# Optimization experiments

Measured on AMD Instinct MI355X. Metric: run time of the kernel, lower is better.

Reference implementation:

```python
import jax, jax.numpy as jnp
import numpy as np

N_BOTTLENECK = 256  # must be a power of two for the butterfly network


def butterfly_ortho(x, theta, first_output_entry_positive=False):
    """FFT-like butterfly of Givens rotations over the last dim (size n, power of 2).
    Stage s pairs indices (i, i + 2^s); each pair gets one rotation angle.
    theta has (n/2)*log2(n) entries, consumed stage by stage.
    """
    n = x.shape[-1]
    stages = int(np.log2(n))
    idx = 0
    for s in range(stages):
        stride = 1 << s
        nb = n // (2 * stride)
        th = theta[idx: idx + n // 2].reshape(nb, stride)
        idx += n // 2
        xr = x.reshape(-1, nb, 2, stride)  # [B, blocks, half, offset]
        a, b = xr[:, :, 0, :], xr[:, :, 1, :]
        c, sn = jnp.cos(th), jnp.sin(th)
        a2 = c * a - sn * b
        b2 = sn * a + c * b
        x = jnp.stack([a2, b2], axis=2).reshape(-1, n)
    if first_output_entry_positive:
        # convention flag: force sign of first output entry non-negative
        x = x.at[:, 0].set(jnp.abs(x[:, 0]))
    return x


def setup_inputs() -> dict:
    key = jax.random.key(0)
    ks = jax.random.split(key, 12)
    dims = [4096, 1024, 256, 1024, 4096]
    B = 16384

    def w(k, i, o):
        return (jax.random.normal(k, (i, o), dtype=jnp.float32) * (1.0 / np.sqrt(i)))

    inp = {
        "x": jax.random.normal(ks[0], (B, dims[0]), dtype=jnp.float32),
        "enc_w0": w(ks[1], dims[0], dims[1]),
        "enc_b0": jnp.zeros((dims[1],), jnp.float32),
        "enc_w1": w(ks[2], dims[1], dims[2]),
        "enc_b1": jnp.zeros((dims[2],), jnp.float32),
        "theta": jax.random.normal(ks[3], ((dims[2] // 2) * int(np.log2(dims[2])),), dtype=jnp.float32),
        "dec_w0": w(ks[4], dims[2], dims[3]),
        "dec_b0": jnp.zeros((dims[3],), jnp.float32),
        "out_w": w(ks[5], dims[3], dims[4]),
        "out_b": jnp.zeros((dims[4],), jnp.float32),
    }
    return inp


def reference(x, enc_w0, enc_b0, enc_w1, enc_b1, theta, dec_w0, dec_b0, out_w, out_b):
    # encoder: Linear + ReLU stack
    h = jax.nn.relu(x @ enc_w0 + enc_b0)
    h = jax.nn.relu(h @ enc_w1 + enc_b1)
    # orthogonal butterfly network at the bottleneck
    h = butterfly_ortho(h, theta, first_output_entry_positive=False)
    # decoder: Linear + ReLU stack, then plain Linear output layer
    h = jax.nn.relu(h @ dec_w0 + dec_b0)
    out = h @ out_w + out_b
    return out
```

## Files before the change

### kernel.cpp

```cpp
#include <hip/hip_runtime.h>

typedef __attribute__((ext_vector_type(8))) short short8v;
typedef __attribute__((ext_vector_type(4))) float f32x4;
typedef __attribute__((ext_vector_type(4))) unsigned int uint4v;
typedef __attribute__((ext_vector_type(4))) float float4v;

__device__ __forceinline__ unsigned short f2bf(float f) {
  union { float f; unsigned u; } v; v.f = f;
  unsigned r = v.u + 0x7fffu + ((v.u >> 16) & 1u);
  return (unsigned short)(r >> 16);
}
__device__ __forceinline__ float bf2f(unsigned short h) {
  union { unsigned u; float f; } v; v.u = ((unsigned)h) << 16;
  return v.f;
}
__device__ __forceinline__ unsigned pack2(float a, float b) {
  return (unsigned)f2bf(a) | ((unsigned)f2bf(b) << 16);
}

__device__ __forceinline__ void gload_lds16(const void* g, void* l) {
  __builtin_amdgcn_global_load_lds(
      (const __attribute__((address_space(1))) void*)g,
      (__attribute__((address_space(3))) void*)l, 16, 0, 0);
}

#define SBAR() __builtin_amdgcn_s_barrier()
#define LGKM0() do { asm volatile("s_waitcnt lgkmcnt(0)" ::: "memory"); \
                     __builtin_amdgcn_sched_barrier(0); } while (0)
#define VMW4() asm volatile("s_waitcnt vmcnt(4)" ::: "memory")

__global__ void f32_to_bf16(const float* __restrict__ in, unsigned short* __restrict__ out,
                            size_t n8) {
  size_t i = (size_t)blockIdx.x * blockDim.x + threadIdx.x;
  const size_t stride = (size_t)gridDim.x * blockDim.x;
  for (; i < n8; i += stride) {
    const float4v* p = (const float4v*)(in + i * 8);
    float4v a = p[0], b = p[1];
    uint4v r;
    r.x = pack2(a.x, a.y); r.y = pack2(a.z, a.w);
    r.z = pack2(b.x, b.y); r.w = pack2(b.z, b.w);
    *(uint4v*)(out + i * 8) = r;
  }
}

__global__ void transpose_bf16(const float* __restrict__ W, unsigned short* __restrict__ WT,
                               int K, int N) {
  __shared__ float t[32][33];
  const int kb = blockIdx.x * 32, nb = blockIdx.y * 32;
  const int tx = threadIdx.x, ty = threadIdx.y;
  #pragma unroll
  for (int y = 0; y < 4; ++y)
    t[ty + y*8][tx] = W[(size_t)(kb + ty + y*8) * N + nb + tx];
  __syncthreads();
  #pragma unroll
  for (int y = 0; y < 4; ++y) {
    const int n = nb + ty + y*8;
    WT[(size_t)n * K + kb + tx] = f2bf(t[tx][ty + y*8]);
  }
}

__global__ void trig_kernel(const float* __restrict__ theta, float* __restrict__ ct,
                            float* __restrict__ st, int n) {
  const int i = blockIdx.x * 256 + threadIdx.x;
  if (i < n) {
    float s, c;
    sincosf(theta[i], &s, &c);
    ct[i] = c; st[i] = s;
  }
}

__global__ void butterfly_kernel(const unsigned short* __restrict__ X,
                                 unsigned short* __restrict__ Y,
                                 const float* __restrict__ ct, const float* __restrict__ st) {
  __shared__ float L[2][256];
  const int tid = threadIdx.x;
  const size_t base = (size_t)blockIdx.x * 512;
  const unsigned v = *(const unsigned*)(X + base + tid * 2);
  const int r = tid >> 7;
  const int col = (tid * 2) & 255;
  L[r][col]     = bf2f((unsigned short)(v & 0xffffu));
  L[r][col + 1] = bf2f((unsigned short)(v >> 16));
  __syncthreads();
  const int p = tid & 127;
  #pragma unroll
  for (int s = 0; s < 8; ++s) {
    const int stride = 1 << s;
    const int t = p & (stride - 1);
    const int i = ((p >> s) << (s + 1)) + t;
    const int j = i + stride;
    const float c  = ct[s * 128 + p];
    const float sn = st[s * 128 + p];
    const float a = L[r][i], b = L[r][j];
    L[r][i] = c * a - sn * b;
    L[r][j] = sn * a + c * b;
    __syncthreads();
  }
  const unsigned lo = f2bf(L[r][col]);
  const unsigned hi = f2bf(L[r][col + 1]);
  *(unsigned*)(Y + base + tid * 2) = lo | (hi << 16);
}

template<bool RELU, bool OUT_F32>
__global__ __launch_bounds__(256) void gemm_kernel(
    const unsigned short* __restrict__ A, const unsigned short* __restrict__ BT,
    const float* __restrict__ bias, void* __restrict__ Cp,
    int M, int N, int K)
{
  __shared__ __align__(16) unsigned short As[128 * 32];
  __shared__ __align__(16) unsigned short Bs[128 * 32];
  const int tid = threadIdx.x;
  const int lane = tid & 63;
  const int w = tid >> 6;
  const int wm = w >> 1, wn = w & 1;
  const int n0 = blockIdx.x * 128;
  const int m0 = blockIdx.y * 128;
  const int g4 = lane >> 4;
  const int ml = lane & 15;

  f32x4 acc[4][4];
  #pragma unroll
  for (int i = 0; i < 4; ++i)
    #pragma unroll
    for (int n = 0; n < 4; ++n)
      #pragma unroll
      for (int e = 0; e < 4; ++e)
        acc[i][n][e] = 0.0f;

  const int nkt = K >> 5;
  const int srow = w * 32 + (lane >> 2);
  const int scol = (lane & 3) * 8;

  for (int kt = 0; kt < nkt; ++kt) {
    const int k0 = kt << 5;
    #pragma unroll
    for (int q = 0; q < 2; ++q) {
      const unsigned short* gb = BT + (size_t)(n0 + srow + q * 16) * K + k0 + scol;
      gload_lds16(gb, Bs + w * 1024 + q * 512);
      const unsigned short* ga = A + (size_t)(m0 + srow + q * 16) * K + k0 + scol;
      gload_lds16(ga, As + w * 1024 + q * 512);
    }
    __syncthreads();
    short8v af[4], bf[4];
    #pragma unroll
    for (int i = 0; i < 4; ++i)
      af[i] = *(const short8v*)(As + (wm * 64 + i * 16 + ml) * 32 + g4 * 8);
    #pragma unroll
    for (int n = 0; n < 4; ++n)
      bf[n] = *(const short8v*)(Bs + (wn * 64 + n * 16 + ml) * 32 + g4 * 8);
    #pragma unroll
    for (int i = 0; i < 4; ++i)
      #pragma unroll
      for (int n = 0; n < 4; ++n)
        acc[i][n] = __builtin_amdgcn_mfma_f32_16x16x32_bf16(af[i], bf[n], acc[i][n], 0, 0, 0);
    __syncthreads();
  }
  #pragma unroll
  for (int n = 0; n < 4; ++n) {
    const int col = n0 + wn * 64 + n * 16 + ml;
    const float bv = bias[col];
    #pragma unroll
    for (int i = 0; i < 4; ++i) {
      const int rowb = m0 + wm * 64 + i * 16 + g4 * 4;
      #pragma unroll
      for (int r = 0; r < 4; ++r) {
        float v = acc[i][n][r] + bv;
        if constexpr (RELU) v = fmaxf(v, 0.0f);
        if constexpr (OUT_F32)
          ((float*)Cp)[(size_t)(rowb + r) * N + col] = v;
        else
          ((unsigned short*)Cp)[(size_t)(rowb + r) * N + col] = f2bf(v);
      }
    }
  }
}

template<int MI0, int NI0>
__device__ __forceinline__ void mfma_quad(f32x4 (&acc)[8][4], const short8v (&a)[4][2],
                                          const short8v (&b)[2][2]) {
  __builtin_amdgcn_s_setprio(1);
  #pragma unroll
  for (int mi = 0; mi < 4; ++mi)
    #pragma unroll
    for (int ni = 0; ni < 2; ++ni) {
      acc[MI0+mi][NI0+ni] = __builtin_amdgcn_mfma_f32_16x16x32_bf16(
          a[mi][0], b[ni][0], acc[MI0+mi][NI0+ni], 0, 0, 0);
      acc[MI0+mi][NI0+ni] = __builtin_amdgcn_mfma_f32_16x16x32_bf16(
          a[mi][1], b[ni][1], acc[MI0+mi][NI0+ni], 0, 0, 0);
    }
  __builtin_amdgcn_s_setprio(0);
}

template<bool RELU, bool OUT_F32>
__global__ __launch_bounds__(512, 2) void gemm256(
    const unsigned short* __restrict__ A, const unsigned short* __restrict__ BT,
    const float* __restrict__ bias, void* __restrict__ Cp,
    int M, int N, int K)
{
  __shared__ __align__(16) unsigned char lds[131072];
  const int tid = threadIdx.x;
  const int lane = tid & 63, w = tid >> 6;
  const int wm = w >> 2, wn = w & 3;
  const int ml = lane & 15, g4 = lane >> 4;

  const int nx = gridDim.x;
  const int nwg = nx * (int)gridDim.y;
  const int bid = blockIdx.y * nx + blockIdx.x;
  const int cpx = nwg >> 3;
  const int swz = (bid & 7) * cpx + (bid >> 3);
  const int n0 = (swz % nx) * 256;
  const int m0 = (swz / nx) * 256;

  const int rloc = w * 8 + (lane >> 3);
  const int scol = ((lane & 7) ^ (lane >> 3)) * 8;
  const int ldst = w * 1024;

  const int off0 = (g4 * 16) ^ ((ml & 7) << 4);
  const int aoff = (wm * 128 + ml) * 128 + off0;
  const int boff = (wn * 64 + ml) * 128 + off0;

  const int NT = K >> 6;
  const int NJ = NT >> 1;

  f32x4 acc[8][4];
  #pragma unroll
  for (int mi = 0; mi < 8; ++mi)
    #pragma unroll
    for (int ni = 0; ni < 4; ++ni)
      #pragma unroll
      for (int e = 0; e < 4; ++e)
        acc[mi][ni][e] = 0.0f;

  auto stA = [&](int d, int h, int t) {
    const unsigned short* g0 = A + (size_t)(m0 + h * 128 + rloc) * K + t * 64 + scol;
    unsigned char* l0 = lds + d * 65536 + h * 16384 + ldst;
    gload_lds16(g0, l0);
    gload_lds16(g0 + (size_t)64 * K, l0 + 8192);
  };
  auto stB = [&](int d, int h, int t) {
    const unsigned short* g0 = BT + (size_t)(n0 + h * 128 + rloc) * K + t * 64 + scol;
    unsigned char* l0 = lds + d * 65536 + 32768 + h * 16384 + ldst;
    gload_lds16(g0, l0);
    gload_lds16(g0 + (size_t)64 * K, l0 + 8192);
  };
  auto rdA = [&](short8v (&dst)[4][2], int d, int mh) {
    #pragma unroll
    for (int mi = 0; mi < 4; ++mi) {
      const int ab = d * 65536 + aoff + (mh * 4 + mi) * 2048;
      dst[mi][0] = *(const short8v*)(lds + ab);
      dst[mi][1] = *(const short8v*)(lds + (ab ^ 64));
    }
  };
  auto rdB = [&](short8v (&dst)[2][2], int d, int nh) {
    #pragma unroll
    for (int ni = 0; ni < 2; ++ni) {
      const int bb = d * 65536 + 32768 + boff + (nh * 2 + ni) * 2048;
      dst[ni][0] = *(const short8v*)(lds + bb);
      dst[ni][1] = *(const short8v*)(lds + (bb ^ 64));
    }
  };

  stB(0, 0, 0); stB(0, 1, 0); stA(0, 0, 0); stA(0, 1, 0);
  stB(1, 0, 1); stB(1, 1, 1);
  VMW4();
  SBAR();

  short8v aR[4][2], aR2[4][2], bR0[2][2], bR1[2][2];

  for (int j = 0; j < NJ; ++j) {
    const int t1 = 2 * j + 1;
    const int t2 = (2 * j + 2 < NT) ? 2 * j + 2 : NT - 1;
    const int t3 = (2 * j + 3 < NT) ? 2 * j + 3 : NT - 1;

    rdA(aR, 0, 0); rdB(bR0, 0, 0);
    stA(1, 0, t1);
    SBAR(); LGKM0();
    mfma_quad<0, 0>(acc, aR, bR0);
    SBAR();
    rdB(bR1, 0, 1);
    stA(1, 1, t1);
    SBAR(); LGKM0();
    mfma_quad<0, 2>(acc, aR, bR1);
    SBAR();
    rdA(aR2, 0, 1);
    stB(0, 0, t2);
    SBAR(); LGKM0();
    mfma_quad<4, 0>(acc, aR2, bR0);
    SBAR();
    stB(0, 1, t2);
    SBAR();
    mfma_quad<4, 2>(acc, aR2, bR1);
    VMW4();
    SBAR();
    rdA(aR, 1, 0); rdB(bR0, 1, 0);
    stA(0, 0, t2);
    SBAR(); LGKM0();
    mfma_quad<0, 0>(acc, aR, bR0);
    SBAR();
    rdB(bR1, 1, 1);
    stA(0, 1, t2);
    SBAR(); LGKM0();
    mfma_quad<0, 2>(acc, aR, bR1);
    SBAR();
    rdA(aR2, 1, 1);
    stB(1, 0, t3);
    SBAR(); LGKM0();
    mfma_quad<4, 0>(acc, aR2, bR0);
    SBAR();
    stB(1, 1, t3);
    SBAR();
    mfma_quad<4, 2>(acc, aR2, bR1);
    VMW4();
    SBAR();
  }

  #pragma unroll
  for (int ni = 0; ni < 4; ++ni) {
    const int col = n0 + wn * 64 + ni * 16 + ml;
    const float bv = bias[col];
    #pragma unroll
    for (int mi = 0; mi < 8; ++mi) {
      const int rowb = m0 + wm * 128 + mi * 16 + g4 * 4;
      #pragma unroll
      for (int r = 0; r < 4; ++r) {
        float v = acc[mi][ni][r] + bv;
        if constexpr (RELU) v = fmaxf(v, 0.0f);
        if constexpr (OUT_F32)
          ((float*)Cp)[(size_t)(rowb + r) * N + col] = v;
        else
          ((unsigned short*)Cp)[(size_t)(rowb + r) * N + col] = f2bf(v);
      }
    }
  }
}

extern "C" void kernel_launch(void* const* d_in, const int* in_sizes, int n_in,
                              void* d_out, int out_size, void* d_ws, size_t ws_size,
                              hipStream_t stream) {
  const float* x      = (const float*)d_in[0];
  const float* enc_w0 = (const float*)d_in[1];
  const float* enc_b0 = (const float*)d_in[2];
  const float* enc_w1 = (const float*)d_in[3];
  const float* enc_b1 = (const float*)d_in[4];
  const float* theta  = (const float*)d_in[5];
  const float* dec_w0 = (const float*)d_in[6];
  const float* dec_b0 = (const float*)d_in[7];
  const float* out_w  = (const float*)d_in[8];
  const float* out_b  = (const float*)d_in[9];
  float* out = (float*)d_out;

  char* ws = (char*)d_ws;
  unsigned short* xb  = (unsigned short*)(ws);
  unsigned short* wt0 = (unsigned short*)(ws + 134217728);
  unsigned short* wt1 = (unsigned short*)(ws + 142606336);
  unsigned short* wt2 = (unsigned short*)(ws + 143130624);
  unsigned short* wt3 = (unsigned short*)(ws + 143654912);
  unsigned short* h1  = (unsigned short*)(ws + 152043520);
  unsigned short* h2  = (unsigned short*)(ws + 185597952);
  unsigned short* h2b = (unsigned short*)(ws + 193986560);
  unsigned short* h3  = h1;
  float* ct = (float*)(ws + 202375168);
  float* st = ct + 1024;

  const int B = 16384;

  f32_to_bf16<<<2048, 256, 0, stream>>>(x, xb, (size_t)B * 4096 / 8);
  transpose_bf16<<<dim3(4096/32, 1024/32), dim3(32, 8), 0, stream>>>(enc_w0, wt0, 4096, 1024);
  transpose_bf16<<<dim3(1024/32,  256/32), dim3(32, 8), 0, stream>>>(enc_w1, wt1, 1024, 256);
  transpose_bf16<<<dim3( 256/32, 1024/32), dim3(32, 8), 0, stream>>>(dec_w0, wt2, 256, 1024);
  transpose_bf16<<<dim3(1024/32, 4096/32), dim3(32, 8), 0, stream>>>(out_w,  wt3, 1024, 4096);
  trig_kernel<<<4, 256, 0, stream>>>(theta, ct, st, 1024);

  gemm256<true,  false><<<dim3(1024/256, B/256), 512, 0, stream>>>(xb, wt0, enc_b0, h1, B, 1024, 4096);
  gemm_kernel<true,  false><<<dim3( 256/128, B/128), 256, 0, stream>>>(h1, wt1, enc_b1, h2, B, 256, 1024);
  butterfly_kernel<<<B/2, 256, 0, stream>>>(h2, h2b, ct, st);
  gemm_kernel<true,  false><<<dim3(1024/128, B/128), 256, 0, stream>>>(h2b, wt2, dec_b0, h3, B, 1024, 256);
  gemm256<false, true ><<<dim3(4096/256, B/256), 512, 0, stream>>>(h3, wt3, out_b, out, B, 4096, 1024);
}
```

Measured before the change: 431.1 us.

## Software-pipeline LDS fragment reads one phase ahead of MFMA in GEMM loop

Restructures the GEMM main loop so LDS reads for the next MFMA quad are issued before the current quad runs. Partial lgkmcnt waits replace full drains, and the vmcnt wait moves earlier so the reads for the next buffer overlap with the last MFMA of the current buffer. The aim is to hide LDS read latency behind matrix math. In exchange, the waitcnt values must exactly match the number of outstanding LDS ops, which risks subtle races, and the fragments read ahead add register pressure.

```diff
diff --git a/kernel.cpp b/kernel.cpp
--- a/kernel.cpp
+++ b/kernel.cpp
@@ -25,9 +25,9 @@
 }
 
 #define SBAR() __builtin_amdgcn_s_barrier()
-#define LGKM0() do { asm volatile("s_waitcnt lgkmcnt(0)" ::: "memory"); \
+#define LGKM(n) do { asm volatile("s_waitcnt lgkmcnt(" #n ")" ::: "memory"); \
                      __builtin_amdgcn_sched_barrier(0); } while (0)
-#define VMW4() asm volatile("s_waitcnt vmcnt(4)" ::: "memory")
+#define VMW(n) asm volatile("s_waitcnt vmcnt(" #n ")" ::: "memory")
 
 __global__ void f32_to_bf16(const float* __restrict__ in, unsigned short* __restrict__ out,
                             size_t n8) {
@@ -259,57 +259,58 @@
     }
   };
 
+  short8v A0[4][2], A1[4][2], B0[2][2], B1[2][2];
+
   stB(0, 0, 0); stB(0, 1, 0); stA(0, 0, 0); stA(0, 1, 0);
   stB(1, 0, 1); stB(1, 1, 1);
-  VMW4();
+  VMW(4);
   SBAR();
-
-  short8v aR[4][2], aR2[4][2], bR0[2][2], bR1[2][2];
+  rdA(A0, 0, 0); rdB(B0, 0, 0);
 
   for (int j = 0; j < NJ; ++j) {
     const int t1 = 2 * j + 1;
     const int t2 = (2 * j + 2 < NT) ? 2 * j + 2 : NT - 1;
     const int t3 = (2 * j + 3 < NT) ? 2 * j + 3 : NT - 1;
 
-    rdA(aR, 0, 0); rdB(bR0, 0, 0);
+    rdB(B1, 0, 1);
     stA(1, 0, t1);
-    SBAR(); LGKM0();
-    mfma_quad<0, 0>(acc, aR, bR0);
-    SBAR();
-    rdB(bR1, 0, 1);
+    SBAR(); LGKM(4);
+    mfma_quad<0, 0>(acc, A0, B0);
+    SBAR();
+    rdA(A1, 0, 1);
     stA(1, 1, t1);
-    SBAR(); LGKM0();
-    mfma_quad<0, 2>(acc, aR, bR1);
-    SBAR();
-    rdA(aR2, 0, 1);
+    SBAR(); LGKM(8);
+    mfma_quad<0, 2>(acc, A0, B1);
+    SBAR();
     stB(0, 0, t2);
-    SBAR(); LGKM0();
-    mfma_quad<4, 0>(acc, aR2, bR0);
-    SBAR();
+    SBAR(); LGKM(0);
+    mfma_quad<4, 0>(acc, A1, B0);
+    VMW(2);
+    SBAR();
+    rdA(A0, 1, 0); rdB(B0, 1, 0);
     stB(0, 1, t2);
-    SBAR();
-    mfma_quad<4, 2>(acc, aR2, bR1);
-    VMW4();
-    SBAR();
-    rdA(aR, 1, 0); rdB(bR0, 1, 0);
+    SBAR(); LGKM(12);
+    mfma_quad<4, 2>(acc, A1, B1);
+    SBAR();
+    rdB(B1, 1, 1);
     stA(0, 0, t2);
-    SBAR(); LGKM0();
-    mfma_quad<0, 0>(acc, aR, bR0);
-    SBAR();
-    rdB(bR1, 1, 1);
+    SBAR(); LGKM(4);
+    mfma_quad<0, 0>(acc, A0, B0);
+    SBAR();
+    rdA(A1, 1, 1);
     stA(0, 1, t2);
-    SBAR(); LGKM0();
-    mfma_quad<0, 2>(acc, aR, bR1);
-    SBAR();
-    rdA(aR2, 1, 1);
+    SBAR(); LGKM(8);
+    mfma_quad<0, 2>(acc, A0, B1);
+    SBAR();
     stB(1, 0, t3);
-    SBAR(); LGKM0();
-    mfma_quad<4, 0>(acc, aR2, bR0);
-    SBAR();
+    SBAR(); LGKM(0);
+    mfma_quad<4, 0>(acc, A1, B0);
+    VMW(2);
+    SBAR();
+    rdA(A0, 0, 0); rdB(B0, 0, 0);
     stB(1, 1, t3);
-    SBAR();
-    mfma_quad<4, 2>(acc, aR2, bR1);
-    VMW4();
+    SBAR(); LGKM(12);
+    mfma_quad<4, 2>(acc, A1, B1);
     SBAR();
   }
 
```

Result: slower. 475.8 us (+10.4%).
